# Performance work log

Hardware: AMD Instinct MI355X
Metric: run time of the kernel (lower is better)

Reference implementation:

```python
import jax, jax.numpy as jnp
import numpy as np

B, S, D = 2, 2048, 1024
M = 2048          # d_mlp
E = 8             # num_experts
TOP_K = 2


def setup_inputs() -> dict:
    key = jax.random.key(0)
    ks = jax.random.split(key, 5)
    std = 0.02
    return {
        "residual": jax.random.normal(ks[0], (B, S, D), jnp.float32),
        "W_router": jax.random.normal(ks[1], (D, E), jnp.float32) * std,
        "W_gate": jax.random.normal(ks[2], (E, D, M), jnp.float32) * std,
        "b_gate": jnp.zeros((E, M), jnp.float32),
        "W_up": jax.random.normal(ks[3], (E, D, M), jnp.float32) * std,
        "b_up": jnp.zeros((E, M), jnp.float32),
        "W_out": jax.random.normal(ks[4], (E, M, D), jnp.float32) * std,
        "b_out": jnp.zeros((E, D), jnp.float32),
    }


def reference(residual, W_router, W_gate, b_gate, W_up, b_up, W_out, b_out):
    # --- router: softmax over experts, top-k selection, renormalize ---
    router_logits = jnp.einsum('bsd,de->bse', residual, W_router)
    router_probs = jax.nn.softmax(router_logits, axis=-1)
    top_k_probs, top_k_idx = jax.lax.top_k(router_probs, TOP_K)          # [B,S,K]
    top_k_probs = top_k_probs / (jnp.sum(top_k_probs, -1, keepdims=True) + 1e-8)
    # per-expert combine weight [B,S,E]; top-k indices are unique per token
    one_hot = jax.nn.one_hot(top_k_idx, E, dtype=residual.dtype)          # [B,S,K,E]
    expert_weights = jnp.einsum('bsk,bske->bse', top_k_probs, one_hot)
    # --- each expert runs dense SwiGLU MLP on the FULL batch (compute-then-mask, as in source) ---
    gate = jax.nn.silu(jnp.einsum('bsd,edm->ebsm', residual, W_gate) + b_gate[:, None, None, :])
    up = jnp.einsum('bsd,edm->ebsm', residual, W_up) + b_up[:, None, None, :]
    hidden = gate * up                                                    # [E,B,S,M]
    expert_out = jnp.einsum('ebsm,emd->ebsd', hidden, W_out) + b_out[:, None, None, :]
    # --- weighted combine (weights are zero for non-selected experts) ---
    output = jnp.einsum('bse,ebsd->bsd', expert_weights, expert_out)
    return output
```

## Files before the change

kernel.cpp:

```cpp
#include <hip/hip_runtime.h>
#include <cstdint>
#include <cstddef>

#define TT 4096
#define DD 1024
#define MM 2048
#define EE 8
#define NPAIR 8192

typedef unsigned short u16;
typedef __bf16 bf16x8 __attribute__((ext_vector_type(8)));
typedef float f32x4 __attribute__((ext_vector_type(4)));
typedef __attribute__((address_space(3))) void* lds_vp;
typedef __attribute__((address_space(1))) const void* gbl_cvp;

__device__ __forceinline__ void async16(u16* l, const u16* g) {
  __builtin_amdgcn_global_load_lds((gbl_cvp)(const void*)g, (lds_vp)(void*)l, 16, 0, 0);
}

__device__ __forceinline__ u16 f2bf(float f) {
  uint32_t u = __builtin_bit_cast(uint32_t, f);
  u += 0x7fffu + ((u >> 16) & 1u);
  return (u16)(u >> 16);
}
__device__ __forceinline__ float bf2f(u16 h) {
  uint32_t u = ((uint32_t)h) << 16;
  return __builtin_bit_cast(float, u);
}

__global__ void router_kernel(const float* __restrict__ X, const float* __restrict__ Wr,
                              int* __restrict__ tok_idx, float* __restrict__ wpair) {
  int wave = threadIdx.x >> 6;
  int lane = threadIdx.x & 63;
  int t = blockIdx.x * 4 + wave;
  const float4* x4 = (const float4*)(X + (size_t)t * DD);
  float acc[EE];
#pragma unroll
  for (int e = 0; e < EE; e++) acc[e] = 0.f;
#pragma unroll
  for (int i = 0; i < 4; i++) {
    float4 xv = x4[i * 64 + lane];
    const float4* wr4 = (const float4*)(Wr + (size_t)(i * 256 + lane * 4) * EE);
    float xs[4] = {xv.x, xv.y, xv.z, xv.w};
#pragma unroll
    for (int c = 0; c < 4; c++) {
      float4 wa = wr4[c * 2 + 0];
      float4 wb = wr4[c * 2 + 1];
      acc[0] += xs[c] * wa.x; acc[1] += xs[c] * wa.y;
      acc[2] += xs[c] * wa.z; acc[3] += xs[c] * wa.w;
      acc[4] += xs[c] * wb.x; acc[5] += xs[c] * wb.y;
      acc[6] += xs[c] * wb.z; acc[7] += xs[c] * wb.w;
    }
  }
#pragma unroll
  for (int off = 32; off > 0; off >>= 1)
#pragma unroll
    for (int e = 0; e < EE; e++) acc[e] += __shfl_xor(acc[e], off);
  if (lane == 0) {
    float mx = acc[0];
#pragma unroll
    for (int e = 1; e < EE; e++) mx = fmaxf(mx, acc[e]);
    float p[EE], s = 0.f;
#pragma unroll
    for (int e = 0; e < EE; e++) { p[e] = __expf(acc[e] - mx); s += p[e]; }
    float inv = 1.f / s;
#pragma unroll
    for (int e = 0; e < EE; e++) p[e] *= inv;
    int i0 = 0;
#pragma unroll
    for (int e = 1; e < EE; e++) if (p[e] > p[i0]) i0 = e;
    int i1 = (i0 == 0) ? 1 : 0;
#pragma unroll
    for (int e = 0; e < EE; e++) if (e != i0 && p[e] > p[i1]) i1 = e;
    float denom = p[i0] + p[i1] + 1e-8f;
    tok_idx[t * 2 + 0] = i0;
    tok_idx[t * 2 + 1] = i1;
    wpair[t * 2 + 0] = p[i0] / denom;
    wpair[t * 2 + 1] = p[i1] / denom;
  }
}

__global__ void bucket_kernel(const int* __restrict__ tok_idx, int* __restrict__ offsets,
                              int* __restrict__ bucket) {
  __shared__ int lcnt[EE];
  __shared__ int lcur[EE];
  int tid = threadIdx.x;
  if (tid < EE) lcnt[tid] = 0;
  __syncthreads();
  for (int i = tid; i < NPAIR; i += 1024) atomicAdd(&lcnt[tok_idx[i]], 1);
  __syncthreads();
  if (tid == 0) {
    int s = 0;
    for (int e = 0; e < EE; e++) {
      offsets[e] = s;
      lcur[e] = s;
      s += lcnt[e];
    }
    offsets[EE] = s;
  }
  __syncthreads();
  for (int i = tid; i < NPAIR; i += 1024) {
    int e = tok_idx[i];
    int pos = atomicAdd(&lcur[e], 1);
    bucket[pos] = i;
  }
}

__global__ void cvtx_kernel(const float* __restrict__ X, u16* __restrict__ Xbf) {
  int i = blockIdx.x * 256 + threadIdx.x;
  float4 v = ((const float4*)X)[i];
  ushort4 o;
  o.x = f2bf(v.x); o.y = f2bf(v.y); o.z = f2bf(v.z); o.w = f2bf(v.w);
  ((ushort4*)Xbf)[i] = o;
}

__global__ void transpose_cvt(const float* __restrict__ in, u16* __restrict__ out, int R, int C) {
  __shared__ float tile[32][33];
  int e = blockIdx.z;
  const float* I = in + (size_t)e * R * C;
  u16* O = out + (size_t)e * R * C;
  int c0 = blockIdx.x * 32, r0 = blockIdx.y * 32;
  for (int i = threadIdx.y; i < 32; i += 8)
    tile[i][threadIdx.x] = I[(size_t)(r0 + i) * C + c0 + threadIdx.x];
  __syncthreads();
  for (int i = threadIdx.y; i < 32; i += 8)
    O[(size_t)(c0 + i) * R + r0 + threadIdx.x] = f2bf(tile[threadIdx.x][i]);
}

template <int MODE>
__global__ __launch_bounds__(256)
void moe_gemm(const u16* __restrict__ Aglob, const u16* __restrict__ Wt,
              const float* __restrict__ bias, u16* __restrict__ Hws,
              float* __restrict__ Ypart, const int* __restrict__ offsets,
              const int* __restrict__ bucket, const float* __restrict__ wpair) {
  constexpr int K = (MODE == 2) ? MM : DD;
  constexpr int N = (MODE == 2) ? DD : MM;

  int x = blockIdx.x;
  int expert = -1, row0 = 0, rows = 0;
#pragma unroll 1
  for (int e = 0; e < EE; e++) {
    int o0 = offsets[e], o1 = offsets[e + 1];
    int nt = (o1 - o0 + 127) >> 7;
    if (x < nt) { expert = e; row0 = o0 + (x << 7); rows = min(128, o1 - row0); break; }
    x -= nt;
  }
  if (expert < 0) return;
  int n0 = blockIdx.y * 128;

  __shared__ u16 Alds[128 * 32];
  __shared__ u16 Blds[128 * 32];

  int tid = threadIdx.x;
  int wave = tid >> 6, lane = tid & 63;
  int wm = wave >> 1, wn = wave & 1;
  int quad = lane >> 4, l15 = lane & 15;

  long arow0, arow1;
  {
    int r0l = wave * 32 + (lane >> 2);
    int r1l = r0l + 16;
    int rr0 = min(r0l, rows - 1);
    int rr1 = min(r1l, rows - 1);
    if (MODE == 2) {
      arow0 = (long)(row0 + rr0) * K;
      arow1 = (long)(row0 + rr1) * K;
    } else {
      arow0 = (long)(bucket[row0 + rr0] >> 1) * K;
      arow1 = (long)(bucket[row0 + rr1] >> 1) * K;
    }
  }
  const u16* Wbase = Wt + (size_t)expert * N * K + (size_t)n0 * K;
  int brow = wave * 32 + (lane >> 2);
  int lchunk = (lane & 3) * 8;

  f32x4 acc[4][4];
#pragma unroll
  for (int i = 0; i < 4; i++)
#pragma unroll
    for (int j = 0; j < 4; j++) acc[i][j] = (f32x4){0.f, 0.f, 0.f, 0.f};

  for (int k0 = 0; k0 < K; k0 += 32) {
    async16(&Alds[(wave * 32) * 32], Aglob + arow0 + k0 + lchunk);
    async16(&Alds[(wave * 32 + 16) * 32], Aglob + arow1 + k0 + lchunk);
    async16(&Blds[(wave * 32) * 32], Wbase + (long)brow * K + k0 + lchunk);
    async16(&Blds[(wave * 32 + 16) * 32], Wbase + (long)(brow + 16) * K + k0 + lchunk);
    __syncthreads();
    bf16x8 af[4], bfr[4];
#pragma unroll
    for (int i = 0; i < 4; i++) {
      af[i]  = *(const bf16x8*)&Alds[(wm * 64 + i * 16 + l15) * 32 + quad * 8];
      bfr[i] = *(const bf16x8*)&Blds[(wn * 64 + i * 16 + l15) * 32 + quad * 8];
    }
#pragma unroll
    for (int i = 0; i < 4; i++)
#pragma unroll
      for (int j = 0; j < 4; j++)
        acc[i][j] = __builtin_amdgcn_mfma_f32_16x16x32_bf16(af[i], bfr[j], acc[i][j], 0, 0, 0);
    __syncthreads();
  }

#pragma unroll
  for (int i = 0; i < 4; i++) {
    int lrb = wm * 64 + i * 16 + quad * 4;
#pragma unroll
    for (int j = 0; j < 4; j++) {
      int gc = n0 + wn * 64 + j * 16 + l15;
      float bv = bias[expert * N + gc];
#pragma unroll
      for (int r = 0; r < 4; r++) {
        int lr = lrb + r;
        if (lr < rows) {
          int grow = row0 + lr;
          float v = acc[i][j][r] + bv;
          if (MODE == 0) {
            Hws[(size_t)grow * MM + gc] = f2bf(v);
          } else if (MODE == 1) {
            float u = bf2f(Hws[(size_t)grow * MM + gc]);
            float sg = v / (1.f + __expf(-v));
            Hws[(size_t)grow * MM + gc] = f2bf(sg * u);
          } else {
            int p = bucket[grow];
            float w = wpair[p];
            Ypart[(size_t)p * DD + gc] = w * v;
          }
        }
      }
    }
  }
}

__global__ void combine_kernel(const float* __restrict__ Ypart, float* __restrict__ out) {
  int i = blockIdx.x * 256 + threadIdx.x;
  int t = i >> 8;
  int c4 = i & 255;
  const float4* y0 = (const float4*)(Ypart + (size_t)(2 * t) * DD) + c4;
  const float4* y1 = (const float4*)(Ypart + (size_t)(2 * t + 1) * DD) + c4;
  float4 a = *y0, b = *y1;
  float4 o;
  o.x = a.x + b.x; o.y = a.y + b.y; o.z = a.z + b.z; o.w = a.w + b.w;
  ((float4*)out)[i] = o;
}

extern "C" void kernel_launch(void* const* d_in, const int* in_sizes, int n_in,
                              void* d_out, int out_size, void* d_ws, size_t ws_size,
                              hipStream_t stream) {
  const float* residual = (const float*)d_in[0];
  const float* W_router = (const float*)d_in[1];
  const float* W_gate   = (const float*)d_in[2];
  const float* b_gate   = (const float*)d_in[3];
  const float* W_up     = (const float*)d_in[4];
  const float* b_up     = (const float*)d_in[5];
  const float* W_out    = (const float*)d_in[6];
  const float* b_out    = (const float*)d_in[7];
  float* out = (float*)d_out;

  char* ws = (char*)d_ws;
  int*   tok_idx = (int*)(ws + 0);
  float* wpair   = (float*)(ws + 32768);
  int*   offsets = (int*)(ws + 65536);
  int*   bucket  = (int*)(ws + 65536 + 512);
  u16*   Xbf  = (u16*)(ws + 131072);
  u16*   WtG  = Xbf + (size_t)TT * DD;
  u16*   WtU  = WtG + (size_t)EE * MM * DD;
  u16*   WtO  = WtU + (size_t)EE * MM * DD;
  u16*   Hws  = WtO + (size_t)EE * DD * MM;
  float* Ypart = (float*)(Hws + (size_t)NPAIR * MM);

  cvtx_kernel<<<dim3(TT * DD / 4 / 256), dim3(256), 0, stream>>>(residual, Xbf);
  transpose_cvt<<<dim3(MM / 32, DD / 32, EE), dim3(32, 8), 0, stream>>>(W_gate, WtG, DD, MM);
  transpose_cvt<<<dim3(MM / 32, DD / 32, EE), dim3(32, 8), 0, stream>>>(W_up,   WtU, DD, MM);
  transpose_cvt<<<dim3(DD / 32, MM / 32, EE), dim3(32, 8), 0, stream>>>(W_out,  WtO, MM, DD);
  router_kernel<<<dim3(TT / 4), dim3(256), 0, stream>>>(residual, W_router, tok_idx, wpair);
  bucket_kernel<<<dim3(1), dim3(1024), 0, stream>>>(tok_idx, offsets, bucket);
  moe_gemm<0><<<dim3(72, MM / 128), dim3(256), 0, stream>>>(Xbf, WtU, b_up,  Hws, Ypart, offsets, bucket, wpair);
  moe_gemm<1><<<dim3(72, MM / 128), dim3(256), 0, stream>>>(Xbf, WtG, b_gate, Hws, Ypart, offsets, bucket, wpair);
  moe_gemm<2><<<dim3(72, DD / 128), dim3(256), 0, stream>>>(Hws, WtO, b_out, Hws, Ypart, offsets, bucket, wpair);
  combine_kernel<<<dim3(TT * DD / 4 / 256), dim3(256), 0, stream>>>(Ypart, out);
}
```

Measured before the change: 529.0 us.

## Fuse X conversion into router, widen weight transpose, swizzle LDS, XCD-aware GEMM grid

The bf16 conversion of the input is folded into the router kernel, which removes one launch and one read of the activations. The weight transpose-convert now uses 64x64 tiles with float4 loads and 16-byte stores. The MoE GEMM applies an XOR swizzle to the K-chunk used for LDS loads and reads, which is meant to cut LDS bank conflicts. GEMM blocks are also remapped to a 1D grid decoded so each XCD gets a contiguous range of row tiles, which should improve L2 reuse of weights. The swizzle has to match exactly between the async loads and the fragment reads, or results will be wrong.

```diff
diff --git a/kernel.cpp b/kernel.cpp
--- a/kernel.cpp
+++ b/kernel.cpp
@@ -11,6 +11,7 @@
 typedef unsigned short u16;
 typedef __bf16 bf16x8 __attribute__((ext_vector_type(8)));
 typedef float f32x4 __attribute__((ext_vector_type(4)));
+typedef u16 u16x8 __attribute__((ext_vector_type(8)));
 typedef __attribute__((address_space(3))) void* lds_vp;
 typedef __attribute__((address_space(1))) const void* gbl_cvp;
 
@@ -29,7 +30,8 @@
 }
 
 __global__ void router_kernel(const float* __restrict__ X, const float* __restrict__ Wr,
-                              int* __restrict__ tok_idx, float* __restrict__ wpair) {
+                              int* __restrict__ tok_idx, float* __restrict__ wpair,
+                              u16* __restrict__ Xbf) {
   int wave = threadIdx.x >> 6;
   int lane = threadIdx.x & 63;
   int t = blockIdx.x * 4 + wave;
@@ -40,6 +42,9 @@
 #pragma unroll
   for (int i = 0; i < 4; i++) {
     float4 xv = x4[i * 64 + lane];
+    ushort4 o;
+    o.x = f2bf(xv.x); o.y = f2bf(xv.y); o.z = f2bf(xv.z); o.w = f2bf(xv.w);
+    *(ushort4*)&Xbf[(size_t)t * DD + (size_t)(i * 64 + lane) * 4] = o;
     const float4* wr4 = (const float4*)(Wr + (size_t)(i * 256 + lane * 4) * EE);
     float xs[4] = {xv.x, xv.y, xv.z, xv.w};
 #pragma unroll
@@ -106,26 +111,62 @@
   }
 }
 
-__global__ void cvtx_kernel(const float* __restrict__ X, u16* __restrict__ Xbf) {
-  int i = blockIdx.x * 256 + threadIdx.x;
-  float4 v = ((const float4*)X)[i];
-  ushort4 o;
-  o.x = f2bf(v.x); o.y = f2bf(v.y); o.z = f2bf(v.z); o.w = f2bf(v.w);
-  ((ushort4*)Xbf)[i] = o;
-}
-
-__global__ void transpose_cvt(const float* __restrict__ in, u16* __restrict__ out, int R, int C) {
-  __shared__ float tile[32][33];
+__global__ __launch_bounds__(256)
+void transpose_cvt(const float* __restrict__ in, u16* __restrict__ out, int R, int C) {
+  __shared__ float tile[64][65];
   int e = blockIdx.z;
   const float* I = in + (size_t)e * R * C;
   u16* O = out + (size_t)e * R * C;
-  int c0 = blockIdx.x * 32, r0 = blockIdx.y * 32;
-  for (int i = threadIdx.y; i < 32; i += 8)
-    tile[i][threadIdx.x] = I[(size_t)(r0 + i) * C + c0 + threadIdx.x];
+  int c0 = blockIdx.x * 64, r0 = blockIdx.y * 64;
+  int t = threadIdx.x;
+  {
+    int cq = t & 15;
+    int rb = t >> 4;
+#pragma unroll
+    for (int i = 0; i < 4; i++) {
+      int r = rb + i * 16;
+      float4 v = *(const float4*)&I[(size_t)(r0 + r) * C + c0 + cq * 4];
+      tile[cq * 4 + 0][r] = v.x;
+      tile[cq * 4 + 1][r] = v.y;
+      tile[cq * 4 + 2][r] = v.z;
+      tile[cq * 4 + 3][r] = v.w;
+    }
+  }
   __syncthreads();
-  for (int i = threadIdx.y; i < 32; i += 8)
-    O[(size_t)(c0 + i) * R + r0 + threadIdx.x] = f2bf(tile[threadIdx.x][i]);
-}
+  {
+    int rseg = (t & 7) * 8;
+    int cc = t >> 3;
+#pragma unroll
+    for (int i = 0; i < 2; i++) {
+      int c = cc + i * 32;
+      u16x8 o;
+#pragma unroll
+      for (int k = 0; k < 8; k++) o[k] = f2bf(tile[c][rseg + k]);
+      *(u16x8*)&O[(size_t)(c0 + c) * R + r0 + rseg] = o;
+    }
+  }
+}
+
+__device__ __forceinline__ bool tile_map(const int* __restrict__ offsets, int x,
+                                         int& expert, int& row0, int& rows) {
+  expert = -1;
+#pragma unroll 1
+  for (int e = 0; e < EE; e++) {
+    int o0 = offsets[e], o1 = offsets[e + 1];
+    int nt = (o1 - o0 + 127) >> 7;
+    if (x < nt) { expert = e; row0 = o0 + (x << 7); rows = min(128, o1 - row0); return true; }
+    x -= nt;
+  }
+  return false;
+}
+
+template <int NTLOG2>
+__device__ __forceinline__ void grid_decode(int bid, int& rt, int& n0) {
+  int xcd = bid & 7, slot = bid >> 3;
+  rt = xcd * 9 + (slot >> NTLOG2);
+  n0 = (slot & ((1 << NTLOG2) - 1)) * 128;
+}
+
 
 template <int MODE>
 __global__ __launch_bounds__(256)
@@ -136,17 +177,10 @@
   constexpr int K = (MODE == 2) ? MM : DD;
   constexpr int N = (MODE == 2) ? DD : MM;
 
-  int x = blockIdx.x;
-  int expert = -1, row0 = 0, rows = 0;
-#pragma unroll 1
-  for (int e = 0; e < EE; e++) {
-    int o0 = offsets[e], o1 = offsets[e + 1];
-    int nt = (o1 - o0 + 127) >> 7;
-    if (x < nt) { expert = e; row0 = o0 + (x << 7); rows = min(128, o1 - row0); break; }
-    x -= nt;
-  }
-  if (expert < 0) return;
-  int n0 = blockIdx.y * 128;
+  int rt, n0;
+  grid_decode<(MODE == 2) ? 3 : 4>(blockIdx.x, rt, n0);
+  int expert, row0, rows;
+  if (!tile_map(offsets, rt, expert, row0, rows)) return;
 
   __shared__ u16 Alds[128 * 32];
   __shared__ u16 Blds[128 * 32];
@@ -155,13 +189,14 @@
   int wave = tid >> 6, lane = tid & 63;
   int wm = wave >> 1, wn = wave & 1;
   int quad = lane >> 4, l15 = lane & 15;
+  int swz = ((lane & 3) ^ ((lane >> 3) & 3)) * 8;
+  int rp  = (quad ^ ((l15 >> 1) & 3)) * 8;
 
   long arow0, arow1;
   {
     int r0l = wave * 32 + (lane >> 2);
-    int r1l = r0l + 16;
     int rr0 = min(r0l, rows - 1);
-    int rr1 = min(r1l, rows - 1);
+    int rr1 = min(r0l + 16, rows - 1);
     if (MODE == 2) {
       arow0 = (long)(row0 + rr0) * K;
       arow1 = (long)(row0 + rr1) * K;
@@ -170,33 +205,37 @@
       arow1 = (long)(bucket[row0 + rr1] >> 1) * K;
     }
   }
-  const u16* Wbase = Wt + (size_t)expert * N * K + (size_t)n0 * K;
-  int brow = wave * 32 + (lane >> 2);
-  int lchunk = (lane & 3) * 8;
+  const u16* A0 = Aglob + arow0 + swz;
+  const u16* A1 = Aglob + arow1 + swz;
+  const u16* B0 = Wt + (size_t)expert * N * K + (size_t)n0 * K
+                  + (long)(wave * 32 + (lane >> 2)) * K + swz;
+  const u16* B1 = B0 + 16 * K;
+
+  u16* sA0 = &Alds[(wave * 32) * 32]; u16* sA1 = &Alds[(wave * 32 + 16) * 32];
+  u16* sB0 = &Blds[(wave * 32) * 32]; u16* sB1 = &Blds[(wave * 32 + 16) * 32];
 
   f32x4 acc[4][4];
 #pragma unroll
   for (int i = 0; i < 4; i++)
 #pragma unroll
-    for (int j = 0; j < 4; j++) acc[i][j] = (f32x4){0.f, 0.f, 0.f, 0.f};
+    for (int j = 0; j < 4; j++) acc[i][j] = (f32x4){0, 0, 0, 0};
 
   for (int k0 = 0; k0 < K; k0 += 32) {
-    async16(&Alds[(wave * 32) * 32], Aglob + arow0 + k0 + lchunk);
-    async16(&Alds[(wave * 32 + 16) * 32], Aglob + arow1 + k0 + lchunk);
-    async16(&Blds[(wave * 32) * 32], Wbase + (long)brow * K + k0 + lchunk);
-    async16(&Blds[(wave * 32 + 16) * 32], Wbase + (long)(brow + 16) * K + k0 + lchunk);
+    async16(sA0, A0); async16(sA1, A1);
+    async16(sB0, B0); async16(sB1, B1);
+    A0 += 32; A1 += 32; B0 += 32; B1 += 32;
     __syncthreads();
-    bf16x8 af[4], bfr[4];
+    bf16x8 af[4], bf[4];
 #pragma unroll
     for (int i = 0; i < 4; i++) {
-      af[i]  = *(const bf16x8*)&Alds[(wm * 64 + i * 16 + l15) * 32 + quad * 8];
-      bfr[i] = *(const bf16x8*)&Blds[(wn * 64 + i * 16 + l15) * 32 + quad * 8];
+      af[i] = *(const bf16x8*)&Alds[(wm * 64 + i * 16 + l15) * 32 + rp];
+      bf[i] = *(const bf16x8*)&Blds[(wn * 64 + i * 16 + l15) * 32 + rp];
     }
 #pragma unroll
     for (int i = 0; i < 4; i++)
 #pragma unroll
       for (int j = 0; j < 4; j++)
-        acc[i][j] = __builtin_amdgcn_mfma_f32_16x16x32_bf16(af[i], bfr[j], acc[i][j], 0, 0, 0);
+        acc[i][j] = __builtin_amdgcn_mfma_f32_16x16x32_bf16(af[i], bf[j], acc[i][j], 0, 0, 0);
     __syncthreads();
   }
 
@@ -267,14 +306,13 @@
   u16*   Hws  = WtO + (size_t)EE * DD * MM;
   float* Ypart = (float*)(Hws + (size_t)NPAIR * MM);
 
-  cvtx_kernel<<<dim3(TT * DD / 4 / 256), dim3(256), 0, stream>>>(residual, Xbf);
-  transpose_cvt<<<dim3(MM / 32, DD / 32, EE), dim3(32, 8), 0, stream>>>(W_gate, WtG, DD, MM);
-  transpose_cvt<<<dim3(MM / 32, DD / 32, EE), dim3(32, 8), 0, stream>>>(W_up,   WtU, DD, MM);
-  transpose_cvt<<<dim3(DD / 32, MM / 32, EE), dim3(32, 8), 0, stream>>>(W_out,  WtO, MM, DD);
-  router_kernel<<<dim3(TT / 4), dim3(256), 0, stream>>>(residual, W_router, tok_idx, wpair);
+  router_kernel<<<dim3(TT / 4), dim3(256), 0, stream>>>(residual, W_router, tok_idx, wpair, Xbf);
   bucket_kernel<<<dim3(1), dim3(1024), 0, stream>>>(tok_idx, offsets, bucket);
-  moe_gemm<0><<<dim3(72, MM / 128), dim3(256), 0, stream>>>(Xbf, WtU, b_up,  Hws, Ypart, offsets, bucket, wpair);
-  moe_gemm<1><<<dim3(72, MM / 128), dim3(256), 0, stream>>>(Xbf, WtG, b_gate, Hws, Ypart, offsets, bucket, wpair);
-  moe_gemm<2><<<dim3(72, DD / 128), dim3(256), 0, stream>>>(Hws, WtO, b_out, Hws, Ypart, offsets, bucket, wpair);
+  transpose_cvt<<<dim3(MM / 64, DD / 64, EE), dim3(256), 0, stream>>>(W_gate, WtG, DD, MM);
+  transpose_cvt<<<dim3(MM / 64, DD / 64, EE), dim3(256), 0, stream>>>(W_up,   WtU, DD, MM);
+  transpose_cvt<<<dim3(DD / 64, MM / 64, EE), dim3(256), 0, stream>>>(W_out,  WtO, MM, DD);
+  moe_gemm<0><<<dim3(8 * 9 * 16), dim3(256), 0, stream>>>(Xbf, WtU, b_up,   Hws, Ypart, offsets, bucket, wpair);
+  moe_gemm<1><<<dim3(8 * 9 * 16), dim3(256), 0, stream>>>(Xbf, WtG, b_gate, Hws, Ypart, offsets, bucket, wpair);
+  moe_gemm<2><<<dim3(8 * 9 * 8),  dim3(256), 0, stream>>>(Hws, WtO, b_out,  Hws, Ypart, offsets, bucket, wpair);
   combine_kernel<<<dim3(TT * DD / 4 / 256), dim3(256), 0, stream>>>(Ypart, out);
 }
```

After: 479.2 us. 1.1x faster.
